# Kernel optimization log

Measured on AMD Instinct MI355X. Metric: run time of the kernel, lower is better.

## Reference

```python
import jax, jax.numpy as jnp
import numpy as np

NUM_HEADS = 16
ALPHA = 1.0          # attention_logits_alpha
SOFTCAP = 50.0       # logit_softcapping


def setup_inputs() -> dict:
    key = jax.random.key(0)
    ks = jax.random.split(key, 7)
    B, S, E = 2, 2048, 2048
    mk = lambda k, shape, sc=1.0: jax.random.normal(k, shape, dtype=jnp.float32) * sc
    return {
        "q": mk(ks[0], (B, S, E)),
        "k": mk(ks[1], (B, S, E)),
        "v": mk(ks[2], (B, S, E)),
        # nn.Linear weights are [out, in]; xavier-ish scale 1/sqrt(E)
        "Wq": mk(ks[3], (E, E), E ** -0.5),
        "Wk": mk(ks[4], (E, E), E ** -0.5),
        "Wv": mk(ks[5], (E, E), E ** -0.5),
        "Wo": mk(ks[6], (E, E), E ** -0.5),
    }


def reference(q, k, v, Wq, Wk, Wv, Wo):
    B, S, E = q.shape
    H = NUM_HEADS
    D = E // H  # head_dim = 128

    def split_heads(x):  # [B,S,E] -> [B,H,S,D]
        return x.reshape(B, S, H, D).transpose(0, 2, 1, 3)

    qh = split_heads(q @ Wq.T)  # q_projection_scale = 1.0
    kh = split_heads(k @ Wk.T)
    vh = split_heads(v @ Wv.T)

    # scaled_dot_product: scale q by 1/sqrt(head_dim)
    qh = qh * (D ** -0.5)
    logits = ALPHA * jnp.einsum("bhqd,bhkd->bhqk", qh, kh)
    # logit softcapping: cap * tanh(logits / cap)
    logits = SOFTCAP * jnp.tanh(logits / SOFTCAP)
    # fp32 softmax (softmax_dtype_fp32=True)
    probs = jax.nn.softmax(logits.astype(jnp.float32), axis=-1).astype(qh.dtype)
    # dropout rate 0.0 -> identity
    ctx = jnp.einsum("bhqk,bhkd->bhqd", probs, vh)
    ctx = ctx.transpose(0, 2, 1, 3).reshape(B, S, E)
    return ctx @ Wo.T  # output_projection_scale = 1.0
```

## Files before the change

### kernel.cpp

```cpp
#include <hip/hip_runtime.h>
#include <hip/hip_bf16.h>
#include <stdint.h>


typedef __attribute__((ext_vector_type(8))) short s16x8;
typedef __attribute__((ext_vector_type(4))) float f32x4;

typedef const __attribute__((address_space(1))) char* gcptr;
typedef __attribute__((address_space(3))) char* lcptr;

#define MFMA_BF16(a, b, c) __builtin_amdgcn_mfma_f32_16x16x32_bf16((a), (b), (c), 0, 0, 0)

__device__ __forceinline__ short f2bf(float f) {
  union { float f; unsigned u; } x; x.f = f;
  unsigned r = (x.u + 0x7fffu + ((x.u >> 16) & 1u)) >> 16;
  return (short)r;
}

__device__ __forceinline__ void gload16(const void* g, void* lds) {
  __builtin_amdgcn_global_load_lds((gcptr)g, (lcptr)lds, 16, 0, 0);
}

constexpr int GK = 2048;
constexpr int SL = 2048, EMB = 2048, HD = 128;

__global__ void cvt_all(const float* __restrict__ q, const float* __restrict__ k,
                        const float* __restrict__ v, const float* __restrict__ wq,
                        const float* __restrict__ wk, const float* __restrict__ wv,
                        const float* __restrict__ wo, short* __restrict__ dst) {
  const int N8A = 1 << 20, N8W = 1 << 19;
  const int total = 3 * N8A + 4 * N8W;
  int i = blockIdx.x * blockDim.x + threadIdx.x;
  int stride = gridDim.x * blockDim.x;
  for (; i < total; i += stride) {
    const float* src;
    size_t loc;
    if (i < 3 * N8A) {
      int sel = i >> 20;
      loc = (size_t)(i & (N8A - 1));
      src = sel == 0 ? q : (sel == 1 ? k : v);
    } else {
      int w = i - 3 * N8A;
      int sel = w >> 19;
      loc = (size_t)(w & (N8W - 1));
      src = sel == 0 ? wq : (sel == 1 ? wk : (sel == 2 ? wv : wo));
    }
    f32x4 a = *reinterpret_cast<const f32x4*>(src + loc * 8);
    f32x4 b = *reinterpret_cast<const f32x4*>(src + loc * 8 + 4);
    s16x8 w8;
#pragma unroll
    for (int j = 0; j < 4; ++j) { w8[j] = f2bf(a[j]); w8[4 + j] = f2bf(b[j]); }
    *reinterpret_cast<s16x8*>(dst + (size_t)i * 8) = w8;
  }
}

template <bool OF32>
__global__ __launch_bounds__(256, 2)
void gemm_bt_bf16(const short* __restrict__ A, const short* __restrict__ B,
                  void* __restrict__ Cv, int gn) {
  __shared__ __align__(16) short As[128 * 64];
  __shared__ __align__(16) short Bs[128 * 64];
  const int tid = threadIdx.x;
  const int lane = tid & 63;
  const int wid = tid >> 6;
  const int wr = wid >> 1, wc = wid & 1;
  const int g = lane >> 4, r = lane & 15;
  const int bm = blockIdx.y, bn = blockIdx.x;

  const f32x4 fz = {0.f, 0.f, 0.f, 0.f};
  f32x4 acc[4][4];
#pragma unroll
  for (int m = 0; m < 4; ++m)
#pragma unroll
    for (int n = 0; n < 4; ++n) acc[m][n] = fz;

  const short* Ab = A + (size_t)bm * 128 * GK;
  const short* Bb = B + (size_t)bn * 128 * GK;

  for (int kt = 0; kt < GK; kt += 64) {
#pragma unroll
    for (int i = 0; i < 4; ++i) {
      int c = i * 256 + tid;
      int row = c >> 3, c8 = c & 7;
      gload16(Ab + (size_t)row * GK + kt + c8 * 8, As + c * 8);
      gload16(Bb + (size_t)row * GK + kt + c8 * 8, Bs + c * 8);
    }
    __syncthreads();
#pragma unroll
    for (int kk = 0; kk < 2; ++kk) {
      s16x8 af[4], bf[4];
#pragma unroll
      for (int m = 0; m < 4; ++m)
        af[m] = *reinterpret_cast<const s16x8*>(As + (wr * 64 + m * 16 + r) * 64 + kk * 32 + g * 8);
#pragma unroll
      for (int n = 0; n < 4; ++n)
        bf[n] = *reinterpret_cast<const s16x8*>(Bs + (wc * 64 + n * 16 + r) * 64 + kk * 32 + g * 8);
#pragma unroll
      for (int m = 0; m < 4; ++m)
#pragma unroll
        for (int n = 0; n < 4; ++n) acc[m][n] = MFMA_BF16(af[m], bf[n], acc[m][n]);
    }
    __syncthreads();
  }

#pragma unroll
  for (int m = 0; m < 4; ++m)
#pragma unroll
    for (int j = 0; j < 4; ++j) {
      int crow = bm * 128 + wr * 64 + m * 16 + g * 4 + j;
      size_t off = (size_t)crow * gn + bn * 128 + wc * 64 + r;
#pragma unroll
      for (int n = 0; n < 4; ++n) {
        if constexpr (OF32) ((float*)Cv)[off + n * 16] = acc[m][n][j];
        else                ((short*)Cv)[off + n * 16] = f2bf(acc[m][n][j]);
      }
    }
}

__global__ __launch_bounds__(256, 2)
void attn(const short* __restrict__ Q, const short* __restrict__ K,
          const short* __restrict__ VT, short* __restrict__ O) {
  __shared__ __align__(16) short Ks[64 * 136];
  __shared__ __align__(16) short Vt[128 * 72];
  __shared__ __align__(16) short Ps[4][2][16 * 72];

  const int tid = threadIdx.x;
  const int lane = tid & 63;
  const int wid = tid >> 6;
  const int g = lane >> 4, r = lane & 15;
  const int qb = blockIdx.x;
  const int bh = blockIdx.y;
  const int b = bh >> 4, h = bh & 15;
  const size_t base = (size_t)b * SL * EMB + (size_t)h * HD;
  const size_t vbase = (size_t)h * HD * 4096 + (size_t)b * SL;

  const int q0 = qb * 128 + wid * 32;
  s16x8 qf[2][4];
#pragma unroll
  for (int s = 0; s < 2; ++s)
#pragma unroll
    for (int kk = 0; kk < 4; ++kk)
      qf[s][kk] = *reinterpret_cast<const s16x8*>(
          Q + base + (size_t)(q0 + s * 16 + r) * EMB + kk * 32 + g * 8);

  const f32x4 fz = {0.f, 0.f, 0.f, 0.f};
  float l_run[2][4];
  f32x4 acc_o[2][8];
#pragma unroll
  for (int s = 0; s < 2; ++s) {
#pragma unroll
    for (int i = 0; i < 4; ++i) l_run[s][i] = 0.f;
#pragma unroll
    for (int i = 0; i < 8; ++i) acc_o[s][i] = fz;
  }

  const float SCALE = 0.08838834764831845f;
  const float C50I = 0.02f;
  const float CA = -1.f / 3.f, CB = 2.f / 15.f;

  const int rk = tid >> 4, ck = tid & 15;
  const int rv = tid >> 3, cv = tid & 7;
  const int cvx = cv ^ (rv & 7);
  s16x8 kreg[4], vreg[4];
#pragma unroll
  for (int i = 0; i < 4; ++i) {
    kreg[i] = *reinterpret_cast<const s16x8*>(K + base + (size_t)(rk + i * 16) * EMB + ck * 8);
    vreg[i] = *reinterpret_cast<const s16x8*>(VT + vbase + (size_t)(rv + i * 32) * 4096 + cv * 8);
  }

  for (int t = 0; t < SL / 64; ++t) {
    __syncthreads();
#pragma unroll
    for (int i = 0; i < 4; ++i) {
      *reinterpret_cast<s16x8*>(&Ks[(rk + i * 16) * 136 + ck * 8]) = kreg[i];
      *reinterpret_cast<s16x8*>(&Vt[(rv + i * 32) * 72 + (cvx << 3)]) = vreg[i];
    }
    __syncthreads();

    if (t + 1 < SL / 64) {
      const int kv1 = (t + 1) * 64;
#pragma unroll
      for (int i = 0; i < 4; ++i) {
        kreg[i] = *reinterpret_cast<const s16x8*>(K + base + (size_t)(kv1 + rk + i * 16) * EMB + ck * 8);
        vreg[i] = *reinterpret_cast<const s16x8*>(VT + vbase + (size_t)(rv + i * 32) * 4096 + kv1 + cv * 8);
      }
    }

    f32x4 sv[2][4];
#pragma unroll
    for (int kn = 0; kn < 4; ++kn) {
      sv[0][kn] = fz; sv[1][kn] = fz;
#pragma unroll
      for (int kk = 0; kk < 4; ++kk) {
        s16x8 kf = *reinterpret_cast<const s16x8*>(&Ks[(kn * 16 + r) * 136 + kk * 32 + g * 8]);
        sv[0][kn] = MFMA_BF16(qf[0][kk], kf, sv[0][kn]);
        sv[1][kn] = MFMA_BF16(qf[1][kk], kf, sv[1][kn]);
      }
    }

#pragma unroll
    for (int s = 0; s < 2; ++s)
#pragma unroll
      for (int kn = 0; kn < 4; ++kn)
#pragma unroll
        for (int reg = 0; reg < 4; ++reg) {
          float z = sv[s][kn][reg] * SCALE;
          float x = z * C50I;
          float x2 = x * x;
          float poly = __builtin_fmaf(x2, __builtin_fmaf(x2, CB, CA), 1.f);
          float cap = fminf(z * poly, 50.f);
          float pe = __expf(cap - 50.f);
          l_run[s][reg] += pe;
          sv[s][kn][reg] = pe;
        }

#pragma unroll
    for (int s = 0; s < 2; ++s)
#pragma unroll
      for (int kn = 0; kn < 4; ++kn)
#pragma unroll
        for (int reg = 0; reg < 4; ++reg)
          Ps[wid][s][(g * 4 + reg) * 72 + kn * 16 + r] = f2bf(sv[s][kn][reg]);

#pragma unroll
    for (int c = 0; c < 2; ++c) {
      s16x8 pa0 = *reinterpret_cast<const s16x8*>(&Ps[wid][0][r * 72 + c * 32 + g * 8]);
      s16x8 pa1 = *reinterpret_cast<const s16x8*>(&Ps[wid][1][r * 72 + c * 32 + g * 8]);
#pragma unroll
      for (int dn = 0; dn < 8; ++dn) {
        int d = dn * 16 + r;
        int pc = ((c * 4 + g) ^ (r & 7));
        s16x8 vf = *reinterpret_cast<const s16x8*>(&Vt[d * 72 + (pc << 3)]);
        acc_o[0][dn] = MFMA_BF16(pa0, vf, acc_o[0][dn]);
        acc_o[1][dn] = MFMA_BF16(pa1, vf, acc_o[1][dn]);
      }
    }
  }

#pragma unroll
  for (int s = 0; s < 2; ++s) {
#pragma unroll
    for (int reg = 0; reg < 4; ++reg) {
#pragma unroll
      for (int off = 1; off < 16; off <<= 1)
        l_run[s][reg] += __shfl_xor(l_run[s][reg], off);
      l_run[s][reg] = 1.f / l_run[s][reg];
    }
#pragma unroll
    for (int dn = 0; dn < 8; ++dn)
#pragma unroll
      for (int reg = 0; reg < 4; ++reg) {
        int row = q0 + s * 16 + g * 4 + reg;
        O[base + (size_t)row * EMB + dn * 16 + r] = f2bf(acc_o[s][dn][reg] * l_run[s][reg]);
      }
  }
}

__global__ void fill_f32(float* p, int n, float val) {
  int i = blockIdx.x * blockDim.x + threadIdx.x;
  if (i < n) p[i] = val;
}

extern "C" void kernel_launch(void* const* d_in, const int* in_sizes, int n_in,
                              void* d_out, int out_size, void* d_ws, size_t ws_size,
                              hipStream_t stream) {
  const float* q  = (const float*)d_in[0];
  const float* k  = (const float*)d_in[1];
  const float* v  = (const float*)d_in[2];
  const float* wq = (const float*)d_in[3];
  const float* wk = (const float*)d_in[4];
  const float* wv = (const float*)d_in[5];
  const float* wo = (const float*)d_in[6];
  float* out = (float*)d_out;

  bool ok = (n_in == 7) && out_size == 8388608;
  for (int i = 0; i < 3 && ok; ++i) ok = (in_sizes[i] == 8388608);
  for (int i = 3; i < 7 && ok; ++i) ok = (in_sizes[i] == 4194304);
  if (!ok) {
    fill_f32<<<(out_size + 255) / 256, 256, 0, stream>>>(out, out_size, 150.f);
    return;
  }

  const size_t NA = 8388608;
  const size_t NW = 4194304;
  const size_t NE = NA;
  const size_t need = (3 * NA + 4 * NW + 4 * NE) * sizeof(short);
  if (ws_size < need) {
    fill_f32<<<(out_size + 255) / 256, 256, 0, stream>>>(out, out_size, 128.f);
    return;
  }

  short* bq  = (short*)d_ws;
  short* bk  = bq + NA;
  short* bv  = bk + NA;
  short* bwq = bv + NA;
  short* bwk = bwq + NW;
  short* bwv = bwk + NW;
  short* bwo = bwv + NW;
  short* Qp  = bwo + NW;
  short* Kp  = Qp + NE;
  short* VpT = Kp + NE;
  short* Cx  = VpT + NE;

  dim3 blk(256);
  dim3 gg(16, 32);
  dim3 ggT(32, 16);
  dim3 ga(SL / 128, 32);

  cvt_all<<<2048, 256, 0, stream>>>(q, k, v, wq, wk, wv, wo, bq);

  gemm_bt_bf16<false><<<gg, blk, 0, stream>>>(bq, bwq, Qp, 2048);
  gemm_bt_bf16<false><<<gg, blk, 0, stream>>>(bk, bwk, Kp, 2048);
  gemm_bt_bf16<false><<<ggT, blk, 0, stream>>>(bwv, bv, VpT, 4096);
  attn<<<ga, blk, 0, stream>>>(Qp, Kp, VpT, Cx);
  gemm_bt_bf16<true><<<gg, blk, 0, stream>>>(Cx, bwo, out, 2048);
}
```

Baseline: 349.8 us.

## Batch QKV GEMMs into one launch and restructure attention with async LDS staging

The three projection GEMMs now run as a single launch that picks operands by blockIdx.z. This cuts launch count and lets the three GEMMs fill the GPU together. The attention kernel moves to 128-key tiles with direct global-to-LDS loads (global_load_lds) using an XOR-swizzled layout. It splits the K and V staging so the next K tile loads during softmax/PV and the next V tile loads during the next QK, and it remaps block indices to group heads. The price is more LDS per block with occupancy dropped to one block per CU, and hand-written waitcnt/barrier sync that must match the load counts.

```diff
diff --git a/kernel.cpp b/kernel.cpp
--- a/kernel.cpp
+++ b/kernel.cpp
@@ -54,10 +54,78 @@
   }
 }
 
-template <bool OF32>
 __global__ __launch_bounds__(256, 2)
-void gemm_bt_bf16(const short* __restrict__ A, const short* __restrict__ B,
-                  void* __restrict__ Cv, int gn) {
+void gemm_qkv(const short* __restrict__ a0, const short* __restrict__ a1,
+              const short* __restrict__ w0, const short* __restrict__ w1,
+              const short* __restrict__ w2, const short* __restrict__ a2,
+              short* __restrict__ o0, short* __restrict__ o1,
+              short* __restrict__ o2) {
+  __shared__ __align__(16) short As[128 * 64];
+  __shared__ __align__(16) short Bs[128 * 64];
+  const int z = blockIdx.z;
+  const short* A = z == 0 ? a0 : (z == 1 ? a1 : w2);
+  const short* B = z == 0 ? w0 : (z == 1 ? w1 : a2);
+  short* C = z == 0 ? o0 : (z == 1 ? o1 : o2);
+  const int bm = z == 2 ? blockIdx.x : blockIdx.y;
+  const int bn = z == 2 ? blockIdx.y : blockIdx.x;
+  const int gn = z == 2 ? 4096 : 2048;
+
+  const int tid = threadIdx.x;
+  const int lane = tid & 63;
+  const int wid = tid >> 6;
+  const int wr = wid >> 1, wc = wid & 1;
+  const int g = lane >> 4, r = lane & 15;
+
+  const f32x4 fz = {0.f, 0.f, 0.f, 0.f};
+  f32x4 acc[4][4];
+#pragma unroll
+  for (int m = 0; m < 4; ++m)
+#pragma unroll
+    for (int n = 0; n < 4; ++n) acc[m][n] = fz;
+
+  const short* Ab = A + (size_t)bm * 128 * GK;
+  const short* Bb = B + (size_t)bn * 128 * GK;
+
+  for (int kt = 0; kt < GK; kt += 64) {
+#pragma unroll
+    for (int i = 0; i < 4; ++i) {
+      int c = i * 256 + tid;
+      int row = c >> 3, c8 = c & 7;
+      gload16(Ab + (size_t)row * GK + kt + c8 * 8, As + c * 8);
+      gload16(Bb + (size_t)row * GK + kt + c8 * 8, Bs + c * 8);
+    }
+    __syncthreads();
+#pragma unroll
+    for (int kk = 0; kk < 2; ++kk) {
+      s16x8 af[4], bf[4];
+#pragma unroll
+      for (int m = 0; m < 4; ++m)
+        af[m] = *reinterpret_cast<const s16x8*>(As + (wr * 64 + m * 16 + r) * 64 + kk * 32 + g * 8);
+#pragma unroll
+      for (int n = 0; n < 4; ++n)
+        bf[n] = *reinterpret_cast<const s16x8*>(Bs + (wc * 64 + n * 16 + r) * 64 + kk * 32 + g * 8);
+#pragma unroll
+      for (int m = 0; m < 4; ++m)
+#pragma unroll
+        for (int n = 0; n < 4; ++n) acc[m][n] = MFMA_BF16(af[m], bf[n], acc[m][n]);
+    }
+    __syncthreads();
+  }
+
+#pragma unroll
+  for (int m = 0; m < 4; ++m)
+#pragma unroll
+    for (int j = 0; j < 4; ++j) {
+      int crow = bm * 128 + wr * 64 + m * 16 + g * 4 + j;
+      size_t off = (size_t)crow * gn + bn * 128 + wc * 64 + r;
+#pragma unroll
+      for (int n = 0; n < 4; ++n) C[off + n * 16] = f2bf(acc[m][n][j]);
+    }
+}
+
+__global__ __launch_bounds__(256, 2)
+void gemm_out(const short* __restrict__ A, const short* __restrict__ B,
+              float* __restrict__ C) {
   __shared__ __align__(16) short As[128 * 64];
   __shared__ __align__(16) short Bs[128 * 64];
   const int tid = threadIdx.x;
@@ -108,28 +176,28 @@
 #pragma unroll
     for (int j = 0; j < 4; ++j) {
       int crow = bm * 128 + wr * 64 + m * 16 + g * 4 + j;
-      size_t off = (size_t)crow * gn + bn * 128 + wc * 64 + r;
-#pragma unroll
-      for (int n = 0; n < 4; ++n) {
-        if constexpr (OF32) ((float*)Cv)[off + n * 16] = acc[m][n][j];
-        else                ((short*)Cv)[off + n * 16] = f2bf(acc[m][n][j]);
-      }
-    }
-}
-
-__global__ __launch_bounds__(256, 2)
+      size_t off = (size_t)crow * 2048 + bn * 128 + wc * 64 + r;
+#pragma unroll
+      for (int n = 0; n < 4; ++n) C[off + n * 16] = acc[m][n][j];
+    }
+}
+
+__global__ __launch_bounds__(256, 1)
 void attn(const short* __restrict__ Q, const short* __restrict__ K,
           const short* __restrict__ VT, short* __restrict__ O) {
-  __shared__ __align__(16) short Ks[64 * 136];
-  __shared__ __align__(16) short Vt[128 * 72];
-  __shared__ __align__(16) short Ps[4][2][16 * 72];
+  __shared__ __align__(16) short Ks[128 * 128];
+  __shared__ __align__(16) short Vt[128 * 128];
+  __shared__ __align__(16) short Ps[4 * 2 * 16 * 136];
 
   const int tid = threadIdx.x;
   const int lane = tid & 63;
   const int wid = tid >> 6;
   const int g = lane >> 4, r = lane & 15;
-  const int qb = blockIdx.x;
-  const int bh = blockIdx.y;
+
+  const int dflat = blockIdx.x + (blockIdx.y << 4);
+  const int cflat = ((dflat & 7) << 6) + (dflat >> 3);
+  const int qb = cflat & 15;
+  const int bh = cflat >> 4;
   const int b = bh >> 4, h = bh & 15;
   const size_t base = (size_t)b * SL * EMB + (size_t)h * HD;
   const size_t vbase = (size_t)h * HD * 4096 + (size_t)b * SL;
@@ -158,50 +226,57 @@
   const float C50I = 0.02f;
   const float CA = -1.f / 3.f, CB = 2.f / 15.f;
 
-  const int rk = tid >> 4, ck = tid & 15;
-  const int rv = tid >> 3, cv = tid & 7;
-  const int cvx = cv ^ (rv & 7);
-  s16x8 kreg[4], vreg[4];
-#pragma unroll
-  for (int i = 0; i < 4; ++i) {
-    kreg[i] = *reinterpret_cast<const s16x8*>(K + base + (size_t)(rk + i * 16) * EMB + ck * 8);
-    vreg[i] = *reinterpret_cast<const s16x8*>(VT + vbase + (size_t)(rv + i * 32) * 4096 + cv * 8);
-  }
-
-  for (int t = 0; t < SL / 64; ++t) {
-    __syncthreads();
-#pragma unroll
-    for (int i = 0; i < 4; ++i) {
-      *reinterpret_cast<s16x8*>(&Ks[(rk + i * 16) * 136 + ck * 8]) = kreg[i];
-      *reinterpret_cast<s16x8*>(&Vt[(rv + i * 32) * 72 + (cvx << 3)]) = vreg[i];
-    }
-    __syncthreads();
-
-    if (t + 1 < SL / 64) {
-      const int kv1 = (t + 1) * 64;
-#pragma unroll
-      for (int i = 0; i < 4; ++i) {
-        kreg[i] = *reinterpret_cast<const s16x8*>(K + base + (size_t)(kv1 + rk + i * 16) * EMB + ck * 8);
-        vreg[i] = *reinterpret_cast<const s16x8*>(VT + vbase + (size_t)(rv + i * 32) * 4096 + kv1 + cv * 8);
-      }
-    }
-
-    f32x4 sv[2][4];
-#pragma unroll
-    for (int kn = 0; kn < 4; ++kn) {
+  const int n0 = (wid << 6) + lane;
+  auto stageK = [&](int t) {
+    const int kv0 = t * 128;
+#pragma unroll
+    for (int i = 0; i < 8; ++i) {
+      int n = n0 + i * 256;
+      int rr = n >> 4, ch = n & 15;
+      int lch = ch ^ (rr & 7);
+      gload16(K + base + (size_t)(kv0 + rr) * EMB + lch * 8, Ks + n * 8);
+    }
+  };
+  auto stageV = [&](int t) {
+    const int kv0 = t * 128;
+#pragma unroll
+    for (int i = 0; i < 8; ++i) {
+      int n = n0 + i * 256;
+      int rr = n >> 4, ch = n & 15;
+      int lch = ch ^ (rr & 7);
+      gload16(VT + vbase + (size_t)rr * 4096 + kv0 + lch * 8, Vt + n * 8);
+    }
+  };
+
+  stageK(0);
+  stageV(0);
+
+  const int psb = (wid * 2) * 16 * 136;
+
+  for (int t = 0; t < SL / 128; ++t) {
+    asm volatile("s_waitcnt vmcnt(8)" ::: "memory");
+    __builtin_amdgcn_s_barrier();
+
+    f32x4 sv[2][8];
+#pragma unroll
+    for (int kn = 0; kn < 8; ++kn) {
       sv[0][kn] = fz; sv[1][kn] = fz;
 #pragma unroll
       for (int kk = 0; kk < 4; ++kk) {
-        s16x8 kf = *reinterpret_cast<const s16x8*>(&Ks[(kn * 16 + r) * 136 + kk * 32 + g * 8]);
+        const s16x8 kf = *reinterpret_cast<const s16x8*>(
+            Ks + ((kn * 16 + r) * 16 + ((kk * 4 + g) ^ (r & 7))) * 8);
         sv[0][kn] = MFMA_BF16(qf[0][kk], kf, sv[0][kn]);
         sv[1][kn] = MFMA_BF16(qf[1][kk], kf, sv[1][kn]);
       }
     }
+    asm volatile("s_waitcnt lgkmcnt(0)" ::: "memory");
+    __builtin_amdgcn_s_barrier();
+    stageK((t + 1) & 15);
 
 #pragma unroll
     for (int s = 0; s < 2; ++s)
 #pragma unroll
-      for (int kn = 0; kn < 4; ++kn)
+      for (int kn = 0; kn < 8; ++kn)
 #pragma unroll
         for (int reg = 0; reg < 4; ++reg) {
           float z = sv[s][kn][reg] * SCALE;
@@ -211,31 +286,33 @@
           float cap = fminf(z * poly, 50.f);
           float pe = __expf(cap - 50.f);
           l_run[s][reg] += pe;
-          sv[s][kn][reg] = pe;
+          Ps[psb + s * 16 * 136 + (g * 4 + reg) * 136 + kn * 16 + r] = f2bf(pe);
         }
 
-#pragma unroll
-    for (int s = 0; s < 2; ++s)
-#pragma unroll
-      for (int kn = 0; kn < 4; ++kn)
-#pragma unroll
-        for (int reg = 0; reg < 4; ++reg)
-          Ps[wid][s][(g * 4 + reg) * 72 + kn * 16 + r] = f2bf(sv[s][kn][reg]);
-
-#pragma unroll
-    for (int c = 0; c < 2; ++c) {
-      s16x8 pa0 = *reinterpret_cast<const s16x8*>(&Ps[wid][0][r * 72 + c * 32 + g * 8]);
-      s16x8 pa1 = *reinterpret_cast<const s16x8*>(&Ps[wid][1][r * 72 + c * 32 + g * 8]);
+    asm volatile("s_waitcnt vmcnt(8)" ::: "memory");
+    __builtin_amdgcn_s_barrier();
+
+#pragma unroll
+    for (int c = 0; c < 4; ++c) {
+      const s16x8 pa0 = *reinterpret_cast<const s16x8*>(
+          Ps + psb + 0 * 16 * 136 + r * 136 + c * 32 + g * 8);
+      const s16x8 pa1 = *reinterpret_cast<const s16x8*>(
+          Ps + psb + 1 * 16 * 136 + r * 136 + c * 32 + g * 8);
 #pragma unroll
       for (int dn = 0; dn < 8; ++dn) {
-        int d = dn * 16 + r;
-        int pc = ((c * 4 + g) ^ (r & 7));
-        s16x8 vf = *reinterpret_cast<const s16x8*>(&Vt[d * 72 + (pc << 3)]);
+        const int d = dn * 16 + r;
+        const s16x8 vf = *reinterpret_cast<const s16x8*>(
+            Vt + (d * 16 + ((c * 4 + g) ^ (r & 7))) * 8);
         acc_o[0][dn] = MFMA_BF16(pa0, vf, acc_o[0][dn]);
         acc_o[1][dn] = MFMA_BF16(pa1, vf, acc_o[1][dn]);
       }
     }
-  }
+    asm volatile("s_waitcnt lgkmcnt(0)" ::: "memory");
+    __builtin_amdgcn_s_barrier();
+    stageV((t + 1) & 15);
+  }
+
+  asm volatile("s_waitcnt vmcnt(0)" ::: "memory");
 
 #pragma unroll
   for (int s = 0; s < 2; ++s) {
@@ -283,8 +360,7 @@
 
   const size_t NA = 8388608;
   const size_t NW = 4194304;
-  const size_t NE = NA;
-  const size_t need = (3 * NA + 4 * NW + 4 * NE) * sizeof(short);
+  const size_t need = (3 * NA + 4 * NW + 4 * NA) * sizeof(short);
   if (ws_size < need) {
     fill_f32<<<(out_size + 255) / 256, 256, 0, stream>>>(out, out_size, 128.f);
     return;
@@ -298,20 +374,17 @@
   short* bwv = bwk + NW;
   short* bwo = bwv + NW;
   short* Qp  = bwo + NW;
-  short* Kp  = Qp + NE;
-  short* VpT = Kp + NE;
-  short* Cx  = VpT + NE;
+  short* Kp  = Qp + NA;
+  short* VpT = Kp + NA;
+  short* Cx  = VpT + NA;
 
   dim3 blk(256);
+  dim3 g3(16, 32, 3);
   dim3 gg(16, 32);
-  dim3 ggT(32, 16);
-  dim3 ga(SL / 128, 32);
+  dim3 ga(16, 32);
 
   cvt_all<<<2048, 256, 0, stream>>>(q, k, v, wq, wk, wv, wo, bq);
-
-  gemm_bt_bf16<false><<<gg, blk, 0, stream>>>(bq, bwq, Qp, 2048);
-  gemm_bt_bf16<false><<<gg, blk, 0, stream>>>(bk, bwk, Kp, 2048);
-  gemm_bt_bf16<false><<<ggT, blk, 0, stream>>>(bwv, bv, VpT, 4096);
+  gemm_qkv<<<g3, blk, 0, stream>>>(bq, bk, bwq, bwk, bwv, bv, Qp, Kp, VpT);
   attn<<<ga, blk, 0, stream>>>(Qp, Kp, VpT, Cx);
-  gemm_bt_bf16<true><<<gg, blk, 0, stream>>>(Cx, bwo, out, 2048);
-}
+  gemm_out<<<gg, blk, 0, stream>>>(Cx, bwo, out);
+}
```

Measured after the change: 378.9 us. 8.3% more time.
